# Optimization experiments

Measured on AMD Instinct MI355X. Metric: run time of the kernel, lower is better.

## Reference

```python
import jax, jax.numpy as jnp
import numpy as np

B, N, C = 4, 2048, 768
H = 6  # 3 obj heads + 3 pose heads (forced by the chained matmul shapes)


def setup_inputs() -> dict:
    key = jax.random.key(0)
    k1, k2, k3 = jax.random.split(key, 3)
    x = jax.random.normal(k1, (B, N, C), dtype=jnp.float32)
    w_qkv = jax.random.normal(k2, (3 * C, C), dtype=jnp.float32) * (C ** -0.5)
    w_proj = jax.random.normal(k3, (C, C // 2), dtype=jnp.float32) * ((C // 2) ** -0.5)
    b_proj = jnp.zeros((C,), dtype=jnp.float32)
    return {"x": x, "w_qkv": w_qkv, "w_proj": w_proj, "b_proj": b_proj, "num_heads": H}


def reference(x, w_qkv, w_proj, b_proj, num_heads):
    b, n, c = x.shape
    hd = c // num_heads
    scale = hd ** -0.5
    # qkv projection -> [3, B, H, N, hd]
    qkv = (x @ w_qkv.T).reshape(b, n, 3, num_heads, hd)
    qkv = jnp.transpose(qkv, (2, 0, 3, 1, 4))
    q, k, v = qkv[0], qkv[1], qkv[2]
    # head split: first 3 heads -> obj (sigmoid), last 3 -> pose (softmax)
    attn_obj = jax.nn.sigmoid(jnp.einsum('bhqd,bhkd->bhqk', q[:, 0:3], k[:, 0:3]) * scale)
    attn_pose = jax.nn.softmax(jnp.einsum('bhqd,bhkd->bhqk', q[:, 3:], k[:, 3:]) * scale, axis=-1)
    # chained matmuls: (attn_pose @ (attn_obj @ v_pose))  -> [B, 3, N, hd]
    ctx = jnp.einsum('bhqk,bhkd->bhqd', attn_obj, v[:, 3:])
    ctx = jnp.einsum('bhqk,bhkd->bhqd', attn_pose, ctx)
    out = jnp.transpose(ctx, (0, 2, 1, 3)).reshape(b, n, c // 2)
    out = out @ w_proj.T + b_proj
    return out, attn_obj
```

## Files before the change

kernel.cpp:

```cpp
#include <hip/hip_runtime.h>

typedef _Float16 half8 __attribute__((ext_vector_type(8)));
typedef _Float16 half4v __attribute__((ext_vector_type(4)));
typedef float f32x4 __attribute__((ext_vector_type(4)));
typedef float f32x16 __attribute__((ext_vector_type(16)));

#define MFMA16(a, b, c) __builtin_amdgcn_mfma_f32_16x16x32_f16((a), (b), (c), 0, 0, 0)
#define MFMA32(a, b, c) __builtin_amdgcn_mfma_f32_32x32x16_f16((a), (b), (c), 0, 0, 0)
#define FENCE() __builtin_amdgcn_sched_barrier(0)
#define BAR() __builtin_amdgcn_s_barrier()

__device__ __forceinline__ void gl_lds16(const void* g, void* l) {
  __builtin_amdgcn_global_load_lds(
      (const __attribute__((address_space(1))) unsigned int*)g,
      (__attribute__((address_space(3))) unsigned int*)l, 16, 0, 0);
}

__device__ __forceinline__ unsigned pkh2(float a, float b) {
  unsigned lo = (unsigned)__builtin_bit_cast(unsigned short, (_Float16)a);
  unsigned hf = (unsigned)__builtin_bit_cast(unsigned short, (_Float16)b);
  return lo | (hf << 16);
}

__global__ __launch_bounds__(256) void k_cvt_all(const float* __restrict__ x,
                                                 const float* __restrict__ wq,
                                                 const float* __restrict__ wp,
                                                 _Float16* __restrict__ xb,
                                                 _Float16* __restrict__ wqb,
                                                 _Float16* __restrict__ wpb) {
  int i = blockIdx.x * 256 + threadIdx.x;
  const float4* src;
  half4v* dst;
  int j;
  if (i < 1572864) { src = (const float4*)x; dst = (half4v*)xb; j = i; }
  else if (i < 1572864 + 442368) { src = (const float4*)wq; dst = (half4v*)wqb; j = i - 1572864; }
  else if (i < 2088960) { src = (const float4*)wp; dst = (half4v*)wpb; j = i - 2015232; }
  else return;
  float4 v = src[j];
  half4v h;
  h[0] = (_Float16)v.x; h[1] = (_Float16)v.y;
  h[2] = (_Float16)v.z; h[3] = (_Float16)v.w;
  dst[j] = h;
}

__global__ __launch_bounds__(256) void k_qkv(const _Float16* __restrict__ A,
                                             const _Float16* __restrict__ Bt,
                                             _Float16* __restrict__ Qw,
                                             _Float16* __restrict__ Kw,
                                             _Float16* __restrict__ Vtw) {
  __shared__ _Float16 As[2][128 * 32];
  __shared__ _Float16 Bs[2][128 * 32];
  const int tid = threadIdx.x;
  const int w = tid >> 6, l = tid & 63;
  const int wr = w >> 1, wc = w & 1;
  const int bid0 = blockIdx.x;
  const int bid = (bid0 & 7) * 144 + (bid0 >> 3);
  const int tm = bid / 18, tn = bid % 18;
  const int m0 = tm * 128, n0 = tn * 128;

  auto stage = [&](int it, int dst) {
    int k0 = it * 32;
#pragma unroll
    for (int r = 0; r < 2; ++r) {
      int seg = r * 256 + tid;
      int row = seg >> 2, cs = seg & 3;
      gl_lds16(A + (size_t)(m0 + row) * 768 + k0 + cs * 8, (char*)As[dst] + (r * 256 + w * 64) * 16);
      gl_lds16(Bt + (size_t)(n0 + row) * 768 + k0 + cs * 8, (char*)Bs[dst] + (r * 256 + w * 64) * 16);
    }
  };

  f32x4 acc[4][4] = {};
  stage(0, 0);
  asm volatile("s_waitcnt vmcnt(0)" ::: "memory");
  BAR();
  for (int it = 0; it < 24; ++it) {
    const int cur = it & 1;
    stage(it + 1, cur ^ 1);
    asm volatile("s_waitcnt vmcnt(4)" ::: "memory");
    FENCE();
    BAR();
    FENCE();
#pragma unroll
    for (int m = 0; m < 4; ++m) {
      half8 av = *(const half8*)&As[cur][(wr * 64 + m * 16 + (l & 15)) * 32 + (l >> 4) * 8];
#pragma unroll
      for (int n = 0; n < 4; ++n) {
        half8 bv = *(const half8*)&Bs[cur][(wc * 64 + n * 16 + (l & 15)) * 32 + (l >> 4) * 8];
        acc[m][n] = MFMA16(av, bv, acc[m][n]);
      }
    }
    FENCE();
    BAR();
  }
  asm volatile("s_waitcnt vmcnt(0)" ::: "memory");

  const float scale = 0.08838834764831845f;
#pragma unroll
  for (int m = 0; m < 4; ++m) {
    int gmb = m0 + wr * 64 + m * 16 + ((l >> 4) << 2);
#pragma unroll
    for (int n = 0; n < 4; ++n) {
      int gn0 = n0 + wc * 64 + n * 16;
      int t = gn0 / 768, rem = gn0 % 768;
      int h = rem >> 7, d = (rem & 127) + (l & 15);
      if (t == 2) {
        int bB = gmb >> 11, ntok0 = gmb & 2047;
        half4v hv;
#pragma unroll
        for (int j = 0; j < 4; ++j) hv[j] = (_Float16)acc[m][n][j];
        *(half4v*)&Vtw[((size_t)(bB * 6 + h) * 128 + d) * 2048 + ntok0] = hv;
      } else {
#pragma unroll
        for (int j = 0; j < 4; ++j) {
          int gm = gmb + j;
          int b = gm >> 11, ntok = gm & 2047;
          float v = acc[m][n][j];
          if (t == 0)
            Qw[((size_t)(b * 6 + h) * 2048 + ntok) * 128 + d] = (_Float16)(v * scale);
          else
            Kw[((size_t)(b * 6 + h) * 2048 + ntok) * 128 + d] = (_Float16)v;
        }
      }
    }
  }
}

__global__ __launch_bounds__(256, 2) void k_obj(const _Float16* __restrict__ Qw,
                                                const _Float16* __restrict__ Kw,
                                                const _Float16* __restrict__ Vtw,
                                                float* __restrict__ attn,
                                                _Float16* __restrict__ c1t) {
  __shared__ _Float16 Ks[2][64 * 128];
  __shared__ _Float16 Vs[2][128 * 64];
  __shared__ float Ts[4][1024];
  const int tid = threadIdx.x, w = tid >> 6, l = tid & 63;
  const int wr = w >> 1, wc = w & 1, hi = l >> 5, q = l & 31;
  const int bid0 = blockIdx.x;
  const int bid = (bid0 & 7) * 48 + (bid0 >> 3);
  const int b = bid / 96, rem = bid % 96, h = rem / 32, qb = rem % 32;
  const _Float16* Qg = Qw + ((size_t)(b * 6 + h) * 2048 + qb * 64 + wr * 32) * 128;
  const _Float16* Kg = Kw + ((size_t)(b * 6 + h) * 2048) * 128;
  const _Float16* Vg = Vtw + ((size_t)(b * 6 + (h + 3)) * 128) * 2048;
  float* attng = attn + ((size_t)(b * 3 + h) * 2048 + qb * 64) * 2048;

  auto stage = [&](int t, int dst) {
#pragma unroll
    for (int r = 0; r < 4; ++r) {
      int seg = r * 256 + tid;
      int row = seg >> 4, cs = (seg & 15) ^ (row & 7);
      gl_lds16(Kg + (size_t)(t * 64 + row) * 128 + cs * 8, (char*)Ks[dst] + (r * 256 + w * 64) * 16);
      int rowv = seg >> 3, csv = (seg & 7) ^ (rowv & 7);
      gl_lds16(Vg + (size_t)rowv * 2048 + t * 64 + csv * 8, (char*)Vs[dst] + (r * 256 + w * 64) * 16);
    }
  };

  half8 qreg[8];
#pragma unroll
  for (int s = 0; s < 8; ++s)
    qreg[s] = *(const half8*)&Qg[(size_t)q * 128 + s * 16 + hi * 8];
  stage(0, 0);
  asm volatile("s_waitcnt vmcnt(0)" ::: "memory");
  BAR();

  f32x16 acc[4] = {};
  for (int kt = 0; kt < 32; ++kt) {
    const int cur = kt & 1;
    stage(kt + 1, cur ^ 1);
    asm volatile("s_waitcnt vmcnt(12)" ::: "memory");
    FENCE();
    BAR();
    FENCE();
    f32x16 p = {};
    const int krow = wc * 32 + q;
    __builtin_amdgcn_s_setprio(1);
#pragma unroll
    for (int s = 0; s < 8; ++s) {
      int chunk = (s * 2 + hi) ^ (krow & 7);
      half8 av = *(const half8*)&Ks[cur][krow * 128 + chunk * 8];
      p = MFMA32(av, qreg[s], p);
    }
    __builtin_amdgcn_s_setprio(0);
    float pf[16];
#pragma unroll
    for (int r = 0; r < 16; ++r) pf[r] = 1.0f / (1.0f + __expf(-p[r]));
    float* T = Ts[w];
#pragma unroll
    for (int r = 0; r < 16; ++r) {
      int kv = (r & 3) + 8 * (r >> 2) + 4 * hi;
      T[q * 32 + (kv ^ ((q & 7) << 2))] = pf[r];
    }
#pragma unroll
    for (int i = 0; i < 4; ++i) {
      int qr = (l >> 3) + 8 * i;
      int kvq = (l & 7) * 4;
      f32x4 v4 = *(const f32x4*)&T[qr * 32 + (kvq ^ ((qr & 7) << 2))];
      *(f32x4*)&attng[(size_t)(wr * 32 + qr) * 2048 + kt * 64 + wc * 32 + kvq] = v4;
    }
#pragma unroll
    for (int ks = 0; ks < 2; ++ks) {
      int r0 = ks * 8;
      unsigned pk01 = pkh2(pf[r0 + 0], pf[r0 + 1]);
      unsigned pk23 = pkh2(pf[r0 + 2], pf[r0 + 3]);
      unsigned pk45 = pkh2(pf[r0 + 4], pf[r0 + 5]);
      unsigned pk67 = pkh2(pf[r0 + 6], pf[r0 + 7]);
      unsigned x = hi ? pk01 : pk45;
      unsigned y = hi ? pk23 : pk67;
      unsigned xsw = (unsigned)__shfl_xor((int)x, 32);
      unsigned ysw = (unsigned)__shfl_xor((int)y, 32);
      union { unsigned u[4]; half8 v; } bf;
      bf.u[0] = hi ? xsw : pk01;
      bf.u[1] = hi ? ysw : pk23;
      bf.u[2] = hi ? pk45 : xsw;
      bf.u[3] = hi ? pk67 : ysw;
      __builtin_amdgcn_s_setprio(1);
#pragma unroll
      for (int dt = 0; dt < 4; ++dt) {
        int vrow = dt * 32 + q;
        int chunk = (wc * 4 + ks * 2 + hi) ^ (vrow & 7);
        half8 av = *(const half8*)&Vs[cur][vrow * 64 + chunk * 8];
        acc[dt] = MFMA32(av, bf.v, acc[dt]);
      }
      __builtin_amdgcn_s_setprio(0);
    }
    FENCE();
    BAR();
  }
  __syncthreads();
  float* mb = (float*)Ks;
  if (wc == 1) {
#pragma unroll
    for (int dt = 0; dt < 4; ++dt)
#pragma unroll
      for (int r = 0; r < 16; ++r) {
        int d = dt * 32 + (r & 3) + 8 * (r >> 2) + 4 * hi;
        mb[(wr * 128 + d) * 32 + q] = acc[dt][r];
      }
  }
  __syncthreads();
  if (wc == 0) {
    _Float16* cg = c1t + (size_t)(b * 3 + h) * 128 * 2048;
    int n = qb * 64 + wr * 32 + q;
#pragma unroll
    for (int dt = 0; dt < 4; ++dt)
#pragma unroll
      for (int r = 0; r < 16; ++r) {
        int d = dt * 32 + (r & 3) + 8 * (r >> 2) + 4 * hi;
        cg[(size_t)d * 2048 + n] = (_Float16)(acc[dt][r] + mb[(wr * 128 + d) * 32 + q]);
      }
  }
}

__global__ __launch_bounds__(256, 2) void k_pose(const _Float16* __restrict__ Qw,
                                                 const _Float16* __restrict__ Kw,
                                                 const _Float16* __restrict__ c1t,
                                                 _Float16* __restrict__ c2) {
  __shared__ _Float16 Ks[2][64 * 128];
  __shared__ _Float16 Cs[2][128 * 64];
  const int tid = threadIdx.x, w = tid >> 6, l = tid & 63;
  const int wr = w >> 1, wc = w & 1, hi = l >> 5, q = l & 31;
  const int bid0 = blockIdx.x;
  const int bid = (bid0 & 7) * 48 + (bid0 >> 3);
  const int b = bid / 96, rem = bid % 96, h = rem / 32, qb = rem % 32;
  const _Float16* Qg = Qw + ((size_t)(b * 6 + h + 3) * 2048 + qb * 64 + wr * 32) * 128;
  const _Float16* Kg = Kw + ((size_t)(b * 6 + h + 3) * 2048) * 128;
  const _Float16* Cg = c1t + ((size_t)(b * 3 + h) * 128) * 2048;

  auto stage = [&](int t, int dst) {
#pragma unroll
    for (int r = 0; r < 4; ++r) {
      int seg = r * 256 + tid;
      int row = seg >> 4, cs = (seg & 15) ^ (row & 7);
      gl_lds16(Kg + (size_t)(t * 64 + row) * 128 + cs * 8, (char*)Ks[dst] + (r * 256 + w * 64) * 16);
      int rowv = seg >> 3, csv = (seg & 7) ^ (rowv & 7);
      gl_lds16(Cg + (size_t)rowv * 2048 + t * 64 + csv * 8, (char*)Cs[dst] + (r * 256 + w * 64) * 16);
    }
  };

  half8 qreg[8];
#pragma unroll
  for (int s = 0; s < 8; ++s)
    qreg[s] = *(const half8*)&Qg[(size_t)q * 128 + s * 16 + hi * 8];
  stage(0, 0);
  asm volatile("s_waitcnt vmcnt(0)" ::: "memory");
  BAR();

  f32x16 acc[4] = {};
  float lsum = 0.f;
  for (int kt = 0; kt < 32; ++kt) {
    const int cur = kt & 1;
    stage(kt + 1, cur ^ 1);
    asm volatile("s_waitcnt vmcnt(8)" ::: "memory");
    FENCE();
    BAR();
    FENCE();
    f32x16 p = {};
    const int krow = wc * 32 + q;
    __builtin_amdgcn_s_setprio(1);
#pragma unroll
    for (int s = 0; s < 8; ++s) {
      int chunk = (s * 2 + hi) ^ (krow & 7);
      half8 av = *(const half8*)&Ks[cur][krow * 128 + chunk * 8];
      p = MFMA32(av, qreg[s], p);
    }
    __builtin_amdgcn_s_setprio(0);
    float pf[16];
#pragma unroll
    for (int r = 0; r < 16; ++r) {
      pf[r] = __expf(p[r]);
      lsum += pf[r];
    }
#pragma unroll
    for (int ks = 0; ks < 2; ++ks) {
      int r0 = ks * 8;
      unsigned pk01 = pkh2(pf[r0 + 0], pf[r0 + 1]);
      unsigned pk23 = pkh2(pf[r0 + 2], pf[r0 + 3]);
      unsigned pk45 = pkh2(pf[r0 + 4], pf[r0 + 5]);
      unsigned pk67 = pkh2(pf[r0 + 6], pf[r0 + 7]);
      unsigned x = hi ? pk01 : pk45;
      unsigned y = hi ? pk23 : pk67;
      unsigned xsw = (unsigned)__shfl_xor((int)x, 32);
      unsigned ysw = (unsigned)__shfl_xor((int)y, 32);
      union { unsigned u[4]; half8 v; } bf;
      bf.u[0] = hi ? xsw : pk01;
      bf.u[1] = hi ? ysw : pk23;
      bf.u[2] = hi ? pk45 : xsw;
      bf.u[3] = hi ? pk67 : ysw;
      __builtin_amdgcn_s_setprio(1);
#pragma unroll
      for (int dt = 0; dt < 4; ++dt) {
        int vrow = dt * 32 + q;
        int chunk = (wc * 4 + ks * 2 + hi) ^ (vrow & 7);
        half8 av = *(const half8*)&Cs[cur][vrow * 64 + chunk * 8];
        acc[dt] = MFMA32(av, bf.v, acc[dt]);
      }
      __builtin_amdgcn_s_setprio(0);
    }
    FENCE();
    BAR();
  }
  __syncthreads();
  float lsum2 = lsum + (float)__shfl_xor(lsum, 32);
  float* mb = (float*)Ks;
  float* lb = (float*)Cs;
  _Float16* ob = (_Float16*)Cs + 512;
  if (wc == 1) {
#pragma unroll
    for (int dt = 0; dt < 4; ++dt)
#pragma unroll
      for (int r = 0; r < 16; ++r) {
        int d = dt * 32 + (r & 3) + 8 * (r >> 2) + 4 * hi;
        mb[(wr * 128 + d) * 32 + q] = acc[dt][r];
      }
    if (l < 32) lb[wr * 32 + q] = lsum2;
  }
  __syncthreads();
  if (wc == 0) {
    float inv = 1.0f / (lsum2 + lb[wr * 32 + q]);
    int qbl = wr * 32 + q;
#pragma unroll
    for (int dt = 0; dt < 4; ++dt)
#pragma unroll
      for (int g = 0; g < 4; ++g) {
        int d0 = dt * 32 + 8 * g + 4 * hi;
        float v0 = (acc[dt][4 * g + 0] + mb[(wr * 128 + d0 + 0) * 32 + q]) * inv;
        float v1 = (acc[dt][4 * g + 1] + mb[(wr * 128 + d0 + 1) * 32 + q]) * inv;
        float v2 = (acc[dt][4 * g + 2] + mb[(wr * 128 + d0 + 2) * 32 + q]) * inv;
        float v3 = (acc[dt][4 * g + 3] + mb[(wr * 128 + d0 + 3) * 32 + q]) * inv;
        union { unsigned u[2]; half4v v; } hv;
        hv.u[0] = pkh2(v0, v1);
        hv.u[1] = pkh2(v2, v3);
        int c8 = (d0 >> 2) ^ ((qbl & 7) << 2);
        *(half4v*)&ob[qbl * 128 + c8 * 4] = hv.v;
      }
  }
  __syncthreads();
  {
    _Float16* cg = c2 + ((size_t)b * 2048 + qb * 64) * 384 + h * 128;
    int qbl = tid >> 2;
#pragma unroll
    for (int j = 0; j < 4; ++j) {
      int ii = (tid & 3) + j * 4;
      int c8 = (ii * 2) ^ ((qbl & 7) << 2);
      half8 v = *(const half8*)&ob[qbl * 128 + c8 * 4];
      *(half8*)&cg[(size_t)qbl * 384 + ii * 8] = v;
    }
  }
}

__global__ __launch_bounds__(256) void k_proj(const _Float16* __restrict__ A,
                                              const _Float16* __restrict__ Bt,
                                              const float* __restrict__ bias,
                                              float* __restrict__ out) {
  __shared__ _Float16 As[2][128 * 32];
  __shared__ _Float16 Bs[2][128 * 32];
  const int tid = threadIdx.x;
  const int w = tid >> 6, l = tid & 63;
  const int wr = w >> 1, wc = w & 1;
  const int bid0 = blockIdx.x;
  const int bid = (bid0 & 7) * 48 + (bid0 >> 3);
  const int tm = bid / 6, tn = bid % 6;
  const int m0 = tm * 128, n0 = tn * 128;

  auto stage = [&](int it, int dst) {
    int k0 = it * 32;
#pragma unroll
    for (int r = 0; r < 2; ++r) {
      int seg = r * 256 + tid;
      int row = seg >> 2, cs = seg & 3;
      gl_lds16(A + (size_t)(m0 + row) * 384 + k0 + cs * 8, (char*)As[dst] + (r * 256 + w * 64) * 16);
      gl_lds16(Bt + (size_t)(n0 + row) * 384 + k0 + cs * 8, (char*)Bs[dst] + (r * 256 + w * 64) * 16);
    }
  };

  f32x4 acc[4][4] = {};
  stage(0, 0);
  asm volatile("s_waitcnt vmcnt(0)" ::: "memory");
  BAR();
  for (int it = 0; it < 12; ++it) {
    const int cur = it & 1;
    stage(it + 1, cur ^ 1);
    asm volatile("s_waitcnt vmcnt(4)" ::: "memory");
    FENCE();
    BAR();
    FENCE();
#pragma unroll
    for (int m = 0; m < 4; ++m) {
      half8 av = *(const half8*)&As[cur][(wr * 64 + m * 16 + (l & 15)) * 32 + (l >> 4) * 8];
#pragma unroll
      for (int n = 0; n < 4; ++n) {
        half8 bv = *(const half8*)&Bs[cur][(wc * 64 + n * 16 + (l & 15)) * 32 + (l >> 4) * 8];
        acc[m][n] = MFMA16(av, bv, acc[m][n]);
      }
    }
    FENCE();
    BAR();
  }
  asm volatile("s_waitcnt vmcnt(0)" ::: "memory");

#pragma unroll
  for (int m = 0; m < 4; ++m) {
    int gmb = m0 + wr * 64 + m * 16 + ((l >> 4) << 2);
#pragma unroll
    for (int n = 0; n < 4; ++n) {
      int gn = n0 + wc * 64 + n * 16 + (l & 15);
      float bv = bias[gn];
#pragma unroll
      for (int j = 0; j < 4; ++j) {
        int gm = gmb + j;
        out[(size_t)gm * 768 + gn] = acc[m][n][j] + bv;
      }
    }
  }
}

extern "C" void kernel_launch(void* const* d_in, const int* in_sizes, int n_in,
                              void* d_out, int out_size, void* d_ws, size_t ws_size,
                              hipStream_t stream) {
  const float* x = (const float*)d_in[0];
  const float* wqkv = (const float*)d_in[1];
  const float* wproj = (const float*)d_in[2];
  const float* bproj = (const float*)d_in[3];

  _Float16* xb = (_Float16*)d_ws;
  _Float16* wqkvb = xb + 6291456;
  _Float16* wprojb = wqkvb + 1769472;
  _Float16* Qw = wprojb + 294912;
  _Float16* Kw = Qw + 6291456;
  _Float16* Vtw = Kw + 6291456;
  _Float16* c1t = Vtw + 6291456;
  _Float16* c2 = c1t + 3145728;

  float* out = (float*)d_out;
  float* attn = out + 6291456;

  k_cvt_all<<<8160, 256, 0, stream>>>(x, wqkv, wproj, xb, wqkvb, wprojb);
  k_qkv<<<64 * 18, 256, 0, stream>>>(xb, wqkvb, Qw, Kw, Vtw);
  k_obj<<<384, 256, 0, stream>>>(Qw, Kw, Vtw, attn, c1t);
  k_pose<<<384, 256, 0, stream>>>(Qw, Kw, c1t, c2);
  k_proj<<<384, 256, 0, stream>>>(c2, wprojb, bproj, out);
}
```

Baseline: 219.4 us.

## Split obj/pose attention over two KV halves with fp32 partials and merge kernels

The obj and pose attention kernels now split the key/value range into two halves, doubling the grid from 384 to 768 blocks. Each half writes fp32 partial context (plus partial softmax row sums for pose), and two new elementwise merge kernels sum the halves and convert to fp16. LDS use drops by single-buffering V/C and shrinking the transpose scratch, so launch bounds can request 3 blocks per CU. The trade is extra global traffic for the fp32 partials, two added launches, and a tighter in-loop wait/barrier schedule. The GEMM prefetch index is also clamped so the last iteration no longer loads past the end.

```diff
diff --git a/kernel.cpp b/kernel.cpp
--- a/kernel.cpp
+++ b/kernel.cpp
@@ -75,7 +75,7 @@
   BAR();
   for (int it = 0; it < 24; ++it) {
     const int cur = it & 1;
-    stage(it + 1, cur ^ 1);
+    stage(it < 23 ? it + 1 : 23, cur ^ 1);
     asm volatile("s_waitcnt vmcnt(4)" ::: "memory");
     FENCE();
     BAR();
@@ -125,32 +125,43 @@
   }
 }
 
-__global__ __launch_bounds__(256, 2) void k_obj(const _Float16* __restrict__ Qw,
+__global__ __launch_bounds__(256, 3) void k_obj(const _Float16* __restrict__ Qw,
                                                 const _Float16* __restrict__ Kw,
                                                 const _Float16* __restrict__ Vtw,
                                                 float* __restrict__ attn,
-                                                _Float16* __restrict__ c1t) {
+                                                float* __restrict__ c1p) {
   __shared__ _Float16 Ks[2][64 * 128];
-  __shared__ _Float16 Vs[2][128 * 64];
-  __shared__ float Ts[4][1024];
+  __shared__ _Float16 Vs[128 * 64];
+  __shared__ float Ts[4][256];
   const int tid = threadIdx.x, w = tid >> 6, l = tid & 63;
   const int wr = w >> 1, wc = w & 1, hi = l >> 5, q = l & 31;
   const int bid0 = blockIdx.x;
-  const int bid = (bid0 & 7) * 48 + (bid0 >> 3);
-  const int b = bid / 96, rem = bid % 96, h = rem / 32, qb = rem % 32;
+  const int bid = (bid0 & 7) * 96 + (bid0 >> 3);
+  const int kvh = bid & 1, u = bid >> 1;
+  const int b = u / 96, remu = u % 96, h = remu / 32, qb = remu % 32;
+  const int kvbase = kvh * 1024;
   const _Float16* Qg = Qw + ((size_t)(b * 6 + h) * 2048 + qb * 64 + wr * 32) * 128;
-  const _Float16* Kg = Kw + ((size_t)(b * 6 + h) * 2048) * 128;
-  const _Float16* Vg = Vtw + ((size_t)(b * 6 + (h + 3)) * 128) * 2048;
-  float* attng = attn + ((size_t)(b * 3 + h) * 2048 + qb * 64) * 2048;
-
-  auto stage = [&](int t, int dst) {
+  const _Float16* Kg = Kw + ((size_t)(b * 6 + h) * 2048 + kvbase) * 128;
+  const _Float16* Vg = Vtw + ((size_t)(b * 6 + h + 3) * 128) * 2048 + kvbase;
+  float* attng = attn + ((size_t)(b * 3 + h) * 2048 + qb * 64) * 2048 + kvbase;
+  float* c1g = c1p + ((size_t)(kvh * 12 + b * 3 + h) * 128) * 2048;
+
+  auto stageK = [&](int t, int dstb) {
 #pragma unroll
     for (int r = 0; r < 4; ++r) {
       int seg = r * 256 + tid;
       int row = seg >> 4, cs = (seg & 15) ^ (row & 7);
-      gl_lds16(Kg + (size_t)(t * 64 + row) * 128 + cs * 8, (char*)Ks[dst] + (r * 256 + w * 64) * 16);
-      int rowv = seg >> 3, csv = (seg & 7) ^ (rowv & 7);
-      gl_lds16(Vg + (size_t)rowv * 2048 + t * 64 + csv * 8, (char*)Vs[dst] + (r * 256 + w * 64) * 16);
+      gl_lds16(Kg + (size_t)(t * 64 + row) * 128 + cs * 8,
+               (char*)Ks[dstb] + (r * 256 + w * 64) * 16);
+    }
+  };
+  auto stageV = [&](int t) {
+#pragma unroll
+    for (int r = 0; r < 4; ++r) {
+      int seg = r * 256 + tid;
+      int row = seg >> 3, cs = (seg & 7) ^ (row & 7);
+      gl_lds16(Vg + (size_t)row * 2048 + t * 64 + cs * 8,
+               (char*)Vs + (r * 256 + w * 64) * 16);
     }
   };
 
@@ -158,18 +169,15 @@
 #pragma unroll
   for (int s = 0; s < 8; ++s)
     qreg[s] = *(const half8*)&Qg[(size_t)q * 128 + s * 16 + hi * 8];
-  stage(0, 0);
-  asm volatile("s_waitcnt vmcnt(0)" ::: "memory");
-  BAR();
+  stageK(0, 0);
 
   f32x16 acc[4] = {};
-  for (int kt = 0; kt < 32; ++kt) {
-    const int cur = kt & 1;
-    stage(kt + 1, cur ^ 1);
-    asm volatile("s_waitcnt vmcnt(12)" ::: "memory");
-    FENCE();
-    BAR();
-    FENCE();
+  for (int kt = 0; kt < 16; ++kt) {
+    const int cur = kt & 1, nxt = cur ^ 1;
+    stageV(kt);
+    stageK((kt + 1) & 15, nxt);
+    asm volatile("s_waitcnt vmcnt(8)" ::: "memory");
+    FENCE(); BAR(); FENCE();
     f32x16 p = {};
     const int krow = wc * 32 + q;
     __builtin_amdgcn_s_setprio(1);
@@ -180,47 +188,63 @@
       p = MFMA32(av, qreg[s], p);
     }
     __builtin_amdgcn_s_setprio(0);
-    float pf[16];
-#pragma unroll
-    for (int r = 0; r < 16; ++r) pf[r] = 1.0f / (1.0f + __expf(-p[r]));
-    float* T = Ts[w];
-#pragma unroll
-    for (int r = 0; r < 16; ++r) {
-      int kv = (r & 3) + 8 * (r >> 2) + 4 * hi;
-      T[q * 32 + (kv ^ ((q & 7) << 2))] = pf[r];
-    }
-#pragma unroll
-    for (int i = 0; i < 4; ++i) {
-      int qr = (l >> 3) + 8 * i;
-      int kvq = (l & 7) * 4;
-      f32x4 v4 = *(const f32x4*)&T[qr * 32 + (kvq ^ ((qr & 7) << 2))];
-      *(f32x4*)&attng[(size_t)(wr * 32 + qr) * 2048 + kt * 64 + wc * 32 + kvq] = v4;
-    }
-#pragma unroll
-    for (int ks = 0; ks < 2; ++ks) {
-      int r0 = ks * 8;
-      unsigned pk01 = pkh2(pf[r0 + 0], pf[r0 + 1]);
-      unsigned pk23 = pkh2(pf[r0 + 2], pf[r0 + 3]);
-      unsigned pk45 = pkh2(pf[r0 + 4], pf[r0 + 5]);
-      unsigned pk67 = pkh2(pf[r0 + 6], pf[r0 + 7]);
-      unsigned x = hi ? pk01 : pk45;
-      unsigned y = hi ? pk23 : pk67;
+#pragma unroll
+    for (int r = 0; r < 16; ++r) p[r] = 1.0f / (1.0f + __expf(-p[r]));
+    union { unsigned uu[4]; half8 v; } bf0, bf1;
+    {
+      unsigned pk01 = pkh2(p[0], p[1]), pk23 = pkh2(p[2], p[3]);
+      unsigned pk45 = pkh2(p[4], p[5]), pk67 = pkh2(p[6], p[7]);
+      unsigned x = hi ? pk01 : pk45, y = hi ? pk23 : pk67;
       unsigned xsw = (unsigned)__shfl_xor((int)x, 32);
       unsigned ysw = (unsigned)__shfl_xor((int)y, 32);
-      union { unsigned u[4]; half8 v; } bf;
-      bf.u[0] = hi ? xsw : pk01;
-      bf.u[1] = hi ? ysw : pk23;
-      bf.u[2] = hi ? pk45 : xsw;
-      bf.u[3] = hi ? pk67 : ysw;
-      __builtin_amdgcn_s_setprio(1);
+      bf0.uu[0] = hi ? xsw : pk01; bf0.uu[1] = hi ? ysw : pk23;
+      bf0.uu[2] = hi ? pk45 : xsw; bf0.uu[3] = hi ? pk67 : ysw;
+    }
+    {
+      unsigned pk01 = pkh2(p[8], p[9]), pk23 = pkh2(p[10], p[11]);
+      unsigned pk45 = pkh2(p[12], p[13]), pk67 = pkh2(p[14], p[15]);
+      unsigned x = hi ? pk01 : pk45, y = hi ? pk23 : pk67;
+      unsigned xsw = (unsigned)__shfl_xor((int)x, 32);
+      unsigned ysw = (unsigned)__shfl_xor((int)y, 32);
+      bf1.uu[0] = hi ? xsw : pk01; bf1.uu[1] = hi ? ysw : pk23;
+      bf1.uu[2] = hi ? pk45 : xsw; bf1.uu[3] = hi ? pk67 : ysw;
+    }
+    asm volatile("s_waitcnt vmcnt(4)" ::: "memory");
+    FENCE(); BAR(); FENCE();
+    __builtin_amdgcn_s_setprio(1);
+#pragma unroll
+    for (int ks = 0; ks < 2; ++ks) {
 #pragma unroll
       for (int dt = 0; dt < 4; ++dt) {
         int vrow = dt * 32 + q;
         int chunk = (wc * 4 + ks * 2 + hi) ^ (vrow & 7);
-        half8 av = *(const half8*)&Vs[cur][vrow * 64 + chunk * 8];
-        acc[dt] = MFMA32(av, bf.v, acc[dt]);
-      }
-      __builtin_amdgcn_s_setprio(0);
+        half8 av = *(const half8*)&Vs[vrow * 64 + chunk * 8];
+        acc[dt] = MFMA32(av, ks ? bf1.v : bf0.v, acc[dt]);
+      }
+    }
+    __builtin_amdgcn_s_setprio(0);
+#pragma unroll
+    for (int rho = 0; rho < 4; ++rho) {
+      asm volatile("s_waitcnt lgkmcnt(0)" ::: "memory");
+      FENCE();
+      if ((q >> 3) == rho) {
+        int qr = q & 7;
+#pragma unroll
+        for (int g = 0; g < 4; ++g) {
+          f32x4 vv;
+          vv[0] = p[g * 4 + 0]; vv[1] = p[g * 4 + 1];
+          vv[2] = p[g * 4 + 2]; vv[3] = p[g * 4 + 3];
+          int kv0 = g * 8 + hi * 4;
+          *(f32x4*)&Ts[w][qr * 32 + (kv0 ^ (qr << 2))] = vv;
+        }
+      }
+      asm volatile("s_waitcnt lgkmcnt(0)" ::: "memory");
+      FENCE();
+      {
+        int row = l >> 3, c0 = (l & 7) * 4;
+        f32x4 vv = *(const f32x4*)&Ts[w][row * 32 + (c0 ^ (row << 2))];
+        *(f32x4*)&attng[(size_t)(wr * 32 + rho * 8 + row) * 2048 + kt * 64 + wc * 32 + c0] = vv;
+      }
     }
     FENCE();
     BAR();
@@ -238,41 +262,64 @@
   }
   __syncthreads();
   if (wc == 0) {
-    _Float16* cg = c1t + (size_t)(b * 3 + h) * 128 * 2048;
     int n = qb * 64 + wr * 32 + q;
 #pragma unroll
     for (int dt = 0; dt < 4; ++dt)
 #pragma unroll
       for (int r = 0; r < 16; ++r) {
         int d = dt * 32 + (r & 3) + 8 * (r >> 2) + 4 * hi;
-        cg[(size_t)d * 2048 + n] = (_Float16)(acc[dt][r] + mb[(wr * 128 + d) * 32 + q]);
-      }
-  }
-}
-
-__global__ __launch_bounds__(256, 2) void k_pose(const _Float16* __restrict__ Qw,
+        c1g[(size_t)d * 2048 + n] = acc[dt][r] + mb[(wr * 128 + d) * 32 + q];
+      }
+  }
+}
+
+__global__ __launch_bounds__(256) void k_merge1(const float* __restrict__ c1p,
+                                                _Float16* __restrict__ c1t) {
+  int i = blockIdx.x * 256 + threadIdx.x;
+  f32x4 a = ((const f32x4*)c1p)[i];
+  f32x4 bb = ((const f32x4*)c1p)[i + 786432];
+  half4v hv;
+#pragma unroll
+  for (int j = 0; j < 4; ++j) hv[j] = (_Float16)(a[j] + bb[j]);
+  ((half4v*)c1t)[i] = hv;
+}
+
+__global__ __launch_bounds__(256, 3) void k_pose(const _Float16* __restrict__ Qw,
                                                  const _Float16* __restrict__ Kw,
                                                  const _Float16* __restrict__ c1t,
-                                                 _Float16* __restrict__ c2) {
+                                                 float* __restrict__ p2,
+                                                 float* __restrict__ lsumw) {
   __shared__ _Float16 Ks[2][64 * 128];
-  __shared__ _Float16 Cs[2][128 * 64];
+  __shared__ _Float16 Cs[128 * 64];
+  __shared__ float lbuf[64];
   const int tid = threadIdx.x, w = tid >> 6, l = tid & 63;
   const int wr = w >> 1, wc = w & 1, hi = l >> 5, q = l & 31;
   const int bid0 = blockIdx.x;
-  const int bid = (bid0 & 7) * 48 + (bid0 >> 3);
-  const int b = bid / 96, rem = bid % 96, h = rem / 32, qb = rem % 32;
+  const int bid = (bid0 & 7) * 96 + (bid0 >> 3);
+  const int kvh = bid & 1, u = bid >> 1;
+  const int b = u / 96, remu = u % 96, h = remu / 32, qb = remu % 32;
+  const int kvbase = kvh * 1024;
   const _Float16* Qg = Qw + ((size_t)(b * 6 + h + 3) * 2048 + qb * 64 + wr * 32) * 128;
-  const _Float16* Kg = Kw + ((size_t)(b * 6 + h + 3) * 2048) * 128;
-  const _Float16* Cg = c1t + ((size_t)(b * 3 + h) * 128) * 2048;
-
-  auto stage = [&](int t, int dst) {
+  const _Float16* Kg = Kw + ((size_t)(b * 6 + h + 3) * 2048 + kvbase) * 128;
+  const _Float16* Cg = c1t + ((size_t)(b * 3 + h) * 128) * 2048 + kvbase;
+  float* p2g = p2 + (size_t)kvh * 3145728 + (size_t)b * 2048 * 384;
+
+  auto stageK = [&](int t, int dstb) {
 #pragma unroll
     for (int r = 0; r < 4; ++r) {
       int seg = r * 256 + tid;
       int row = seg >> 4, cs = (seg & 15) ^ (row & 7);
-      gl_lds16(Kg + (size_t)(t * 64 + row) * 128 + cs * 8, (char*)Ks[dst] + (r * 256 + w * 64) * 16);
-      int rowv = seg >> 3, csv = (seg & 7) ^ (rowv & 7);
-      gl_lds16(Cg + (size_t)rowv * 2048 + t * 64 + csv * 8, (char*)Cs[dst] + (r * 256 + w * 64) * 16);
+      gl_lds16(Kg + (size_t)(t * 64 + row) * 128 + cs * 8,
+               (char*)Ks[dstb] + (r * 256 + w * 64) * 16);
+    }
+  };
+  auto stageC = [&](int t) {
+#pragma unroll
+    for (int r = 0; r < 4; ++r) {
+      int seg = r * 256 + tid;
+      int row = seg >> 3, cs = (seg & 7) ^ (row & 7);
+      gl_lds16(Cg + (size_t)row * 2048 + t * 64 + cs * 8,
+               (char*)Cs + (r * 256 + w * 64) * 16);
     }
   };
 
@@ -280,19 +327,16 @@
 #pragma unroll
   for (int s = 0; s < 8; ++s)
     qreg[s] = *(const half8*)&Qg[(size_t)q * 128 + s * 16 + hi * 8];
-  stage(0, 0);
-  asm volatile("s_waitcnt vmcnt(0)" ::: "memory");
-  BAR();
+  stageK(0, 0);
 
   f32x16 acc[4] = {};
   float lsum = 0.f;
-  for (int kt = 0; kt < 32; ++kt) {
-    const int cur = kt & 1;
-    stage(kt + 1, cur ^ 1);
+  for (int kt = 0; kt < 16; ++kt) {
+    const int cur = kt & 1, nxt = cur ^ 1;
+    stageC(kt);
+    stageK((kt + 1) & 15, nxt);
     asm volatile("s_waitcnt vmcnt(8)" ::: "memory");
-    FENCE();
-    BAR();
-    FENCE();
+    FENCE(); BAR(); FENCE();
     f32x16 p = {};
     const int krow = wc * 32 + q;
     __builtin_amdgcn_s_setprio(1);
@@ -303,46 +347,50 @@
       p = MFMA32(av, qreg[s], p);
     }
     __builtin_amdgcn_s_setprio(0);
-    float pf[16];
 #pragma unroll
     for (int r = 0; r < 16; ++r) {
-      pf[r] = __expf(p[r]);
-      lsum += pf[r];
-    }
-#pragma unroll
-    for (int ks = 0; ks < 2; ++ks) {
-      int r0 = ks * 8;
-      unsigned pk01 = pkh2(pf[r0 + 0], pf[r0 + 1]);
-      unsigned pk23 = pkh2(pf[r0 + 2], pf[r0 + 3]);
-      unsigned pk45 = pkh2(pf[r0 + 4], pf[r0 + 5]);
-      unsigned pk67 = pkh2(pf[r0 + 6], pf[r0 + 7]);
-      unsigned x = hi ? pk01 : pk45;
-      unsigned y = hi ? pk23 : pk67;
+      p[r] = __expf(p[r]);
+      lsum += p[r];
+    }
+    union { unsigned uu[4]; half8 v; } bf0, bf1;
+    {
+      unsigned pk01 = pkh2(p[0], p[1]), pk23 = pkh2(p[2], p[3]);
+      unsigned pk45 = pkh2(p[4], p[5]), pk67 = pkh2(p[6], p[7]);
+      unsigned x = hi ? pk01 : pk45, y = hi ? pk23 : pk67;
       unsigned xsw = (unsigned)__shfl_xor((int)x, 32);
       unsigned ysw = (unsigned)__shfl_xor((int)y, 32);
-      union { unsigned u[4]; half8 v; } bf;
-      bf.u[0] = hi ? xsw : pk01;
-      bf.u[1] = hi ? ysw : pk23;
-      bf.u[2] = hi ? pk45 : xsw;
-      bf.u[3] = hi ? pk67 : ysw;
-      __builtin_amdgcn_s_setprio(1);
+      bf0.uu[0] = hi ? xsw : pk01; bf0.uu[1] = hi ? ysw : pk23;
+      bf0.uu[2] = hi ? pk45 : xsw; bf0.uu[3] = hi ? pk67 : ysw;
+    }
+    {
+      unsigned pk01 = pkh2(p[8], p[9]), pk23 = pkh2(p[10], p[11]);
+      unsigned pk45 = pkh2(p[12], p[13]), pk67 = pkh2(p[14], p[15]);
+      unsigned x = hi ? pk01 : pk45, y = hi ? pk23 : pk67;
+      unsigned xsw = (unsigned)__shfl_xor((int)x, 32);
+      unsigned ysw = (unsigned)__shfl_xor((int)y, 32);
+      bf1.uu[0] = hi ? xsw : pk01; bf1.uu[1] = hi ? ysw : pk23;
+      bf1.uu[2] = hi ? pk45 : xsw; bf1.uu[3] = hi ? pk67 : ysw;
+    }
+    asm volatile("s_waitcnt vmcnt(4)" ::: "memory");
+    FENCE(); BAR(); FENCE();
+    __builtin_amdgcn_s_setprio(1);
+#pragma unroll
+    for (int ks = 0; ks < 2; ++ks) {
 #pragma unroll
       for (int dt = 0; dt < 4; ++dt) {
         int vrow = dt * 32 + q;
         int chunk = (wc * 4 + ks * 2 + hi) ^ (vrow & 7);
-        half8 av = *(const half8*)&Cs[cur][vrow * 64 + chunk * 8];
-        acc[dt] = MFMA32(av, bf.v, acc[dt]);
-      }
-      __builtin_amdgcn_s_setprio(0);
-    }
+        half8 av = *(const half8*)&Cs[vrow * 64 + chunk * 8];
+        acc[dt] = MFMA32(av, ks ? bf1.v : bf0.v, acc[dt]);
+      }
+    }
+    __builtin_amdgcn_s_setprio(0);
     FENCE();
     BAR();
   }
   __syncthreads();
   float lsum2 = lsum + (float)__shfl_xor(lsum, 32);
   float* mb = (float*)Ks;
-  float* lb = (float*)Cs;
-  _Float16* ob = (_Float16*)Cs + 512;
   if (wc == 1) {
 #pragma unroll
     for (int dt = 0; dt < 4; ++dt)
@@ -351,40 +399,67 @@
         int d = dt * 32 + (r & 3) + 8 * (r >> 2) + 4 * hi;
         mb[(wr * 128 + d) * 32 + q] = acc[dt][r];
       }
-    if (l < 32) lb[wr * 32 + q] = lsum2;
+    if (hi == 0) lbuf[wr * 32 + q] = lsum2;
   }
   __syncthreads();
+  float* Cf = (float*)Cs;
   if (wc == 0) {
-    float inv = 1.0f / (lsum2 + lb[wr * 32 + q]);
-    int qbl = wr * 32 + q;
 #pragma unroll
     for (int dt = 0; dt < 4; ++dt)
 #pragma unroll
-      for (int g = 0; g < 4; ++g) {
-        int d0 = dt * 32 + 8 * g + 4 * hi;
-        float v0 = (acc[dt][4 * g + 0] + mb[(wr * 128 + d0 + 0) * 32 + q]) * inv;
-        float v1 = (acc[dt][4 * g + 1] + mb[(wr * 128 + d0 + 1) * 32 + q]) * inv;
-        float v2 = (acc[dt][4 * g + 2] + mb[(wr * 128 + d0 + 2) * 32 + q]) * inv;
-        float v3 = (acc[dt][4 * g + 3] + mb[(wr * 128 + d0 + 3) * 32 + q]) * inv;
-        union { unsigned u[2]; half4v v; } hv;
-        hv.u[0] = pkh2(v0, v1);
-        hv.u[1] = pkh2(v2, v3);
-        int c8 = (d0 >> 2) ^ ((qbl & 7) << 2);
-        *(half4v*)&ob[qbl * 128 + c8 * 4] = hv.v;
-      }
-  }
-  __syncthreads();
-  {
-    _Float16* cg = c2 + ((size_t)b * 2048 + qb * 64) * 384 + h * 128;
-    int qbl = tid >> 2;
-#pragma unroll
-    for (int j = 0; j < 4; ++j) {
-      int ii = (tid & 3) + j * 4;
-      int c8 = (ii * 2) ^ ((qbl & 7) << 2);
-      half8 v = *(const half8*)&ob[qbl * 128 + c8 * 4];
-      *(half8*)&cg[(size_t)qbl * 384 + ii * 8] = v;
-    }
-  }
+      for (int r = 0; r < 16; ++r) {
+        int d = dt * 32 + (r & 3) + 8 * (r >> 2) + 4 * hi;
+        acc[dt][r] += mb[(wr * 128 + d) * 32 + q];
+      }
+    float lsump = lsum2 + lbuf[wr * 32 + q];
+    if (hi == 0)
+      lsumw[(size_t)(kvh * 12 + b * 3 + h) * 2048 + qb * 64 + wr * 32 + q] = lsump;
+  }
+#pragma unroll
+  for (int rr = 0; rr < 2; ++rr) {
+    __syncthreads();
+    if (wc == 0 && wr == rr) {
+#pragma unroll
+      for (int dt = 0; dt < 4; ++dt)
+#pragma unroll
+        for (int g = 0; g < 4; ++g) {
+          int d0 = dt * 32 + g * 8 + hi * 4, c = d0 >> 2;
+          f32x4 vv;
+          vv[0] = acc[dt][g * 4 + 0]; vv[1] = acc[dt][g * 4 + 1];
+          vv[2] = acc[dt][g * 4 + 2]; vv[3] = acc[dt][g * 4 + 3];
+          *(f32x4*)&Cf[q * 128 + ((c ^ ((q & 7) << 2)) << 2)] = vv;
+        }
+    }
+    __syncthreads();
+    {
+      int nl = tid >> 3, cbase = (tid & 7) * 4;
+#pragma unroll
+      for (int j = 0; j < 4; ++j) {
+        int c = cbase + j;
+        f32x4 vv = *(const f32x4*)&Cf[nl * 128 + ((c ^ ((nl & 7) << 2)) << 2)];
+        *(f32x4*)&p2g[(size_t)(qb * 64 + rr * 32 + nl) * 384 + h * 128 + (c << 2)] = vv;
+      }
+    }
+  }
+}
+
+__global__ __launch_bounds__(256) void k_merge2(const float* __restrict__ p2,
+                                                const float* __restrict__ lsumw,
+                                                _Float16* __restrict__ c2) {
+  int i = blockIdx.x * 256 + threadIdx.x;
+  size_t i4 = (size_t)i * 4;
+  int n = (int)(i4 / 384);
+  int h = ((int)(i4 % 384)) >> 7;
+  int b = n >> 11, nl = n & 2047;
+  int hh = b * 3 + h;
+  float ls = lsumw[hh * 2048 + nl] + lsumw[24576 + hh * 2048 + nl];
+  float inv = 1.0f / ls;
+  f32x4 a = ((const f32x4*)p2)[i];
+  f32x4 bb = ((const f32x4*)p2)[i + 786432];
+  half4v hv;
+#pragma unroll
+  for (int j = 0; j < 4; ++j) hv[j] = (_Float16)((a[j] + bb[j]) * inv);
+  ((half4v*)c2)[i] = hv;
 }
 
 __global__ __launch_bounds__(256) void k_proj(const _Float16* __restrict__ A,
@@ -418,7 +493,7 @@
   BAR();
   for (int it = 0; it < 12; ++it) {
     const int cur = it & 1;
-    stage(it + 1, cur ^ 1);
+    stage(it < 11 ? it + 1 : 11, cur ^ 1);
     asm volatile("s_waitcnt vmcnt(4)" ::: "memory");
     FENCE();
     BAR();
@@ -469,13 +544,18 @@
   _Float16* Vtw = Kw + 6291456;
   _Float16* c1t = Vtw + 6291456;
   _Float16* c2 = c1t + 3145728;
+  float* c1p = (float*)(c2 + 3145728);
+  float* p2 = c1p + 6291456;
+  float* lsumw = p2 + 6291456;
 
   float* out = (float*)d_out;
   float* attn = out + 6291456;
 
   k_cvt_all<<<8160, 256, 0, stream>>>(x, wqkv, wproj, xb, wqkvb, wprojb);
-  k_qkv<<<64 * 18, 256, 0, stream>>>(xb, wqkvb, Qw, Kw, Vtw);
-  k_obj<<<384, 256, 0, stream>>>(Qw, Kw, Vtw, attn, c1t);
-  k_pose<<<384, 256, 0, stream>>>(Qw, Kw, c1t, c2);
+  k_qkv<<<1152, 256, 0, stream>>>(xb, wqkvb, Qw, Kw, Vtw);
+  k_obj<<<768, 256, 0, stream>>>(Qw, Kw, Vtw, attn, c1p);
+  k_merge1<<<3072, 256, 0, stream>>>(c1p, c1t);
+  k_pose<<<768, 256, 0, stream>>>(Qw, Kw, c1t, p2, lsumw);
+  k_merge2<<<3072, 256, 0, stream>>>(p2, lsumw, c2);
   k_proj<<<384, 256, 0, stream>>>(c2, wprojb, bproj, out);
 }
```

Measured after the change: 216.7 us. Within noise of the previous version (-1.2%).
